# Performance work log

Measured on AMD Instinct MI355X. Metric: run time of the kernel, lower is better.

## Reference

```python
import jax, jax.numpy as jnp
import numpy as np

B = 131072
NUM_KNOTS = 20
X_RANGE = (-5.0, 5.0)
DIMS = [3, 16, 16, 16, 16, 16, 16, 2]
KNOTS = jnp.linspace(X_RANGE[0], X_RANGE[1], NUM_KNOTS, dtype=jnp.float32)


def setup_inputs() -> dict:
    key = jax.random.key(0)
    keys = jax.random.split(key, 2 + 2 * (len(DIMS) - 1))
    inp = {
        "x": jax.random.normal(keys[0], (B, 2), dtype=jnp.float32),
        "t": jax.random.uniform(keys[1], (B, 1), dtype=jnp.float32),
    }
    for l in range(len(DIMS) - 1):
        in_d, out_d = DIMS[l], DIMS[l + 1]
        # per-edge cubic coefficients for each knot interval: [out, in, K-1, 4]
        inp[f"c{l}"] = 0.05 * jax.random.normal(
            keys[2 + 2 * l], (out_d, in_d, NUM_KNOTS - 1, 4), dtype=jnp.float32)
        inp[f"b{l}"] = jnp.zeros((out_d,), dtype=jnp.float32)
    return inp


def kan_layer(x, coeffs, bias):
    """x: [B, in]; coeffs: [out, in, K-1, 4]; bias: [out] -> [B, out].
    Vectorized equivalent of the per-edge CubicSplineFunction double loop:
    bucketize -> gather interval coeffs -> cubic polynomial in dx -> sum over in.
    """
    n_int = coeffs.shape[2]
    idx = jnp.clip(jnp.searchsorted(KNOTS, x, side="right") - 1, 0, n_int - 1)  # [B, in]
    dx = x - KNOTS[idx]                                                          # [B, in]
    dxp = jnp.stack([jnp.ones_like(dx), dx, dx * dx, dx * dx * dx], axis=-1)     # [B, in, 4]
    ii = jnp.arange(x.shape[1])
    cg = coeffs[:, ii[None, :], idx]                                             # [out, B, in, 4]
    return jnp.einsum("obip,bip->bo", cg, dxp) + bias


def reference(x, t, c0, b0, c1, b1, c2, b2, c3, b3, c4, b4, c5, b5, c6, b6):
    cs = [c0, c1, c2, c3, c4, c5, c6]
    bs = [b0, b1, b2, b3, b4, b5, b6]
    h = jnp.concatenate([x, t], axis=1)
    for l in range(len(cs) - 1):
        h = jax.nn.silu(kan_layer(h, cs[l], bs[l]))
    out = kan_layer(h, cs[-1], bs[-1])  # [B, 2]
    return jax.lax.complex(out[..., 0], out[..., 1])
```

## Files before the change

### kernel.cpp

```cpp
#include <hip/hip_runtime.h>
#include <hip/hip_fp16.h>
#include <math.h>


#define B_TOTAL 131072
#define NK 20
#define NI 19

#define W_L0 0
#define W_L1 912
#define W_L6 25232
#define W_TOTAL 25840
#define LSTRIDE 4864

typedef _Float16 h2_t __attribute__((ext_vector_type(2)));

__device__ __forceinline__ h2_t u2h2(unsigned u) {
    union { unsigned u; h2_t h; } c;
    c.u = u;
    return c.h;
}

__device__ __forceinline__ unsigned h2u(h2_t h) {
    union { h2_t h; unsigned u; } c;
    c.h = h;
    return c.u;
}

__device__ __forceinline__ float silu(float a) {
    return a / (1.0f + expf(-a));
}

__device__ __forceinline__ float silu_fast(float a) {
#if __has_builtin(__builtin_amdgcn_rcpf)
    return a * __builtin_amdgcn_rcpf(1.0f + __expf(-a));
#else
    return a / (1.0f + __expf(-a));
#endif
}

__device__ __forceinline__ void find_idx(float v, const float* __restrict__ skp,
                                         int& idx, float& dx) {
    int g0 = (int)floorf((v + 5.0f) * 1.9f);
    g0 = g0 < 0 ? 0 : (g0 > NI - 1 ? NI - 1 : g0);
    const float k0 = skp[g0], k1 = skp[g0 + 1], k2 = skp[g0 + 2];
    int id = g0 - 1; float kk = k0;
    if (v >= k1) { id = g0;     kk = k1; }
    if (v >= k2) { id = g0 + 1; kk = k2; }
    if (id < 0)      { id = 0;      kk = k1; }
    if (id > NI - 1) { id = NI - 1; kk = k1; }
    idx = id; dx = v - kk;
}

#if __has_builtin(__builtin_amdgcn_fdot2)
__device__ __forceinline__ float edge2(unsigned q12, unsigned q03, h2_t dxv,
                                       h2_t onev, float acc) {
    acc = __builtin_amdgcn_fdot2(u2h2(q03), onev, acc, false);
    acc = __builtin_amdgcn_fdot2(u2h2(q12), dxv, acc, false);
    return acc;
}
#else
__device__ __forceinline__ float edge2(unsigned q12, unsigned q03, h2_t dxv,
                                       h2_t onev, float acc) {
    const h2_t a = u2h2(q12), b = u2h2(q03);
    acc += (float)b.x + (float)b.y * (float)onev.y;
    acc += (float)a.x * (float)dxv.x + (float)a.y * (float)dxv.y;
    return acc;
}
#endif

__device__ __forceinline__ float quad_reduce_sum(float v) {
    int t = __builtin_amdgcn_mov_dpp(__float_as_int(v), 0xB1, 0xF, 0xF, true);
    v += __int_as_float(t);
    t = __builtin_amdgcn_mov_dpp(__float_as_int(v), 0x4E, 0xF, 0xF, true);
    v += __int_as_float(t);
    return v;
}

__device__ __forceinline__ void prep_own(float a, const float* __restrict__ skp,
                                         int& mi, unsigned& md, unsigned& mo) {
    const float h = silu_fast(a);
    int idx; float dx;
    find_idx(h, skp, idx, dx);
    const float dx2 = dx * dx, dx3 = dx2 * dx;
    const h2_t dxv = {(_Float16)dx, (_Float16)dx2};
    const h2_t onev = {(_Float16)1.0f, (_Float16)dx3};
    mi = idx; md = h2u(dxv); mo = h2u(onev);
}

template <int HALF>
__device__ __forceinline__ uint4 gl16(const __half* base, unsigned voff) {
    uint4 d;
    if constexpr (HALF == 0)
        asm volatile("global_load_dwordx4 %0, %1, %2 offset:0"
                     : "=v"(d)
                     : "v"(voff), "s"(base));
    else
        asm volatile("global_load_dwordx4 %0, %1, %2 offset:16"
                     : "=v"(d)
                     : "v"(voff), "s"(base));
    return d;
}

#define VM_WAIT_SB(N)                                         \
    do {                                                      \
        asm volatile("s_waitcnt vmcnt(" #N ")" ::: "memory"); \
        __builtin_amdgcn_sched_barrier(0);                    \
    } while (0)

template <int K>
__device__ __forceinline__ void issue_batch(const __half* base, const int* mi,
                                            int q32, uint4* d) {
#pragma unroll
    for (int j = 0; j < 4; ++j) {
        const int idx =
            __builtin_amdgcn_mov_dpp(mi[j], K * 0x55, 0xF, 0xF, true);
        const unsigned voff =
            (unsigned)((((K * 4 + j) * NI + idx) << 7) + q32);
        d[2 * j] = gl16<0>(base, voff);
        d[2 * j + 1] = gl16<1>(base, voff);
    }
}

template <int K>
__device__ __forceinline__ void consume_batch(const uint4* src,
                                              const unsigned* md,
                                              const unsigned* mo, float* acc) {
#pragma unroll
    for (int j = 0; j < 4; ++j) {
        const h2_t dxv = u2h2((unsigned)__builtin_amdgcn_mov_dpp(
            (int)md[j], K * 0x55, 0xF, 0xF, true));
        const h2_t onev = u2h2((unsigned)__builtin_amdgcn_mov_dpp(
            (int)mo[j], K * 0x55, 0xF, 0xF, true));
        const uint4 qa = src[2 * j], qb = src[2 * j + 1];
        acc[0] = edge2(qa.x, qa.y, dxv, onev, acc[0]);
        acc[1] = edge2(qa.z, qa.w, dxv, onev, acc[1]);
        acc[2] = edge2(qb.x, qb.y, dxv, onev, acc[2]);
        acc[3] = edge2(qb.z, qb.w, dxv, onev, acc[3]);
    }
}

__global__ __launch_bounds__(256, 4) void kan_kernel_v6(
    const float* __restrict__ x, const float* __restrict__ t,
    const __half* __restrict__ w, float* __restrict__ out) {
    __shared__ float skp[NK + 1];
    if (threadIdx.x < NK + 1)
        skp[threadIdx.x] =
            (threadIdx.x == 0)
                ? -3.0e38f
                : (float)(-5.0 + (double)(threadIdx.x - 1) * (10.0 / 19.0));
    __syncthreads();

    const int q = threadIdx.x & 3;
    const int q4 = q * 4;
    const int q32 = q4 << 3;
    const int s = blockIdx.x * 64 + (threadIdx.x >> 2);

    const float2 xy = ((const float2*)x)[s];
    const float tv = t[s];

    float acc[4] = {0.f, 0.f, 0.f, 0.f};

    {
        const char* __restrict__ bpq = (const char*)w + q32;
        const float vin[3] = {xy.x, xy.y, tv};
        int i0[3]; unsigned d0[3], o0[3];
#pragma unroll
        for (int i = 0; i < 3; ++i) {
            int idx; float dx;
            find_idx(vin[i], skp, idx, dx);
            const float dx2 = dx * dx, dx3 = dx2 * dx;
            const h2_t dxv = {(_Float16)dx, (_Float16)dx2};
            const h2_t onev = {(_Float16)1.0f, (_Float16)dx3};
            i0[i] = idx; d0[i] = h2u(dxv); o0[i] = h2u(onev);
        }
        uint4 L0[6];
#pragma unroll
        for (int i = 0; i < 3; ++i) {
            const char* p = bpq + (((i * NI) + i0[i]) * 128);
            L0[2 * i] = *(const uint4*)p;
            L0[2 * i + 1] = *(const uint4*)(p + 16);
        }
#pragma unroll
        for (int i = 0; i < 3; ++i) {
            const h2_t dxv = u2h2(d0[i]), onev = u2h2(o0[i]);
            const uint4 qa = L0[2 * i], qb = L0[2 * i + 1];
            acc[0] = edge2(qa.x, qa.y, dxv, onev, acc[0]);
            acc[1] = edge2(qa.z, qa.w, dxv, onev, acc[1]);
            acc[2] = edge2(qb.x, qb.y, dxv, onev, acc[2]);
            acc[3] = edge2(qb.z, qb.w, dxv, onev, acc[3]);
        }
    }

#pragma unroll 1
    for (int l = 0; l < 5; ++l) {
        int mi[4]; unsigned md[4], mo[4];
#pragma unroll
        for (int ii = 0; ii < 4; ++ii)
            prep_own(acc[ii], skp, mi[ii], md[ii], mo[ii]);
#pragma unroll
        for (int j = 0; j < 4; ++j) acc[j] = 0.f;

        const __half* base = w + ((size_t)W_L1 + (size_t)l * LSTRIDE) * 4;

        uint4 b0[8], b1[8], b2[8], b3[8];
        issue_batch<0>(base, mi, q32, b0);
        issue_batch<1>(base, mi, q32, b1);
        VM_WAIT_SB(8);
        consume_batch<0>(b0, md, mo, acc);
        issue_batch<2>(base, mi, q32, b2);
        VM_WAIT_SB(8);
        consume_batch<1>(b1, md, mo, acc);
        issue_batch<3>(base, mi, q32, b3);
        VM_WAIT_SB(8);
        consume_batch<2>(b2, md, mo, acc);
        VM_WAIT_SB(0);
        consume_batch<3>(b3, md, mo, acc);
    }

    {
        const char* __restrict__ c6p = (const char*)w + (size_t)W_L6 * 8;
        int i6[4]; unsigned d6[4], o6[4];
#pragma unroll
        for (int ii = 0; ii < 4; ++ii)
            prep_own(acc[ii], skp, i6[ii], d6[ii], o6[ii]);
        uint4 qv[4];
#pragma unroll
        for (int ii = 0; ii < 4; ++ii)
            qv[ii] = *(const uint4*)(c6p + (((q4 + ii) * NI + i6[ii]) * 16));
        float a0 = 0.f, a1 = 0.f;
#pragma unroll
        for (int ii = 0; ii < 4; ++ii) {
            const h2_t dxv = u2h2(d6[ii]), onev = u2h2(o6[ii]);
            a0 = edge2(qv[ii].x, qv[ii].y, dxv, onev, a0);
            a1 = edge2(qv[ii].z, qv[ii].w, dxv, onev, a1);
        }
        a0 = quad_reduce_sum(a0);
        a1 = quad_reduce_sum(a1);
        if (q == 0) out[s] = a0;
        else if (q == 1) out[B_TOTAL + s] = a1;
    }
}

__global__ __launch_bounds__(256) void repack_kernel(
    const float4* __restrict__ c0, const float4* __restrict__ c1,
    const float4* __restrict__ c2, const float4* __restrict__ c3,
    const float4* __restrict__ c4, const float4* __restrict__ c5,
    const float4* __restrict__ c6, __half* __restrict__ w) {
    const int tid = blockIdx.x * 256 + threadIdx.x;
    if (tid >= W_TOTAL) return;
    const float4* src;
    int IN, OUT, off;
    if (tid < W_L1)                      { src = c0; IN = 3;  OUT = 16; off = W_L0; }
    else if (tid < W_L1 + 1 * LSTRIDE)   { src = c1; IN = 16; OUT = 16; off = W_L1; }
    else if (tid < W_L1 + 2 * LSTRIDE)   { src = c2; IN = 16; OUT = 16; off = W_L1 + 1 * LSTRIDE; }
    else if (tid < W_L1 + 3 * LSTRIDE)   { src = c3; IN = 16; OUT = 16; off = W_L1 + 2 * LSTRIDE; }
    else if (tid < W_L1 + 4 * LSTRIDE)   { src = c4; IN = 16; OUT = 16; off = W_L1 + 3 * LSTRIDE; }
    else if (tid < W_L6)                 { src = c5; IN = 16; OUT = 16; off = W_L1 + 4 * LSTRIDE; }
    else                                 { src = c6; IN = 16; OUT = 2;  off = W_L6; }
    const int d = tid - off;
    const int o = d % OUT;
    const int ik = d / OUT;
    const int k = ik % NI, i = ik / NI;
    const float4 s = src[((size_t)o * IN + i) * NI + k];
    __half* dst = w + (size_t)tid * 4;
    dst[0] = __float2half(s.y);
    dst[1] = __float2half(s.z);
    dst[2] = __float2half(s.x);
    dst[3] = __float2half(s.w);
}

template <int IN, int OUT, bool DO_SILU>
__device__ __forceinline__ void kan_layer_fb(const float* __restrict__ h_in,
                                             float* __restrict__ h_out,
                                             const float4* __restrict__ C,
                                             const float* __restrict__ skp) {
    float acc[OUT];
#pragma unroll
    for (int o = 0; o < OUT; ++o) acc[o] = 0.0f;
#pragma unroll 1
    for (int i = 0; i < IN; ++i) {
        int idx; float dx;
        find_idx(h_in[i], skp, idx, dx);
        const float dx2 = dx * dx, dx3 = dx2 * dx;
        const float4* __restrict__ cp = C + (i * NI + idx);
#pragma unroll
        for (int o = 0; o < OUT; ++o) {
            const float4 c = cp[o * IN * NI];
            acc[o] += fmaf(c.y, dx, fmaf(c.z, dx2, fmaf(c.w, dx3, c.x)));
        }
    }
#pragma unroll
    for (int o = 0; o < OUT; ++o) h_out[o] = DO_SILU ? silu(acc[o]) : acc[o];
}

__global__ __launch_bounds__(256) void kan_kernel_fb(
    const float* __restrict__ x, const float* __restrict__ t,
    const float4* __restrict__ c0, const float4* __restrict__ c1,
    const float4* __restrict__ c2, const float4* __restrict__ c3,
    const float4* __restrict__ c4, const float4* __restrict__ c5,
    const float4* __restrict__ c6, float* __restrict__ out) {
    __shared__ float skp[NK + 1];
    if (threadIdx.x < NK + 1)
        skp[threadIdx.x] =
            (threadIdx.x == 0)
                ? -3.0e38f
                : (float)(-5.0 + (double)(threadIdx.x - 1) * (10.0 / 19.0));
    __syncthreads();
    const int b = blockIdx.x * blockDim.x + threadIdx.x;
    if (b >= B_TOTAL) return;
    const float2 xy = ((const float2*)x)[b];
    float h0[3] = {xy.x, xy.y, t[b]};
    float ha[16], hb[16];
    kan_layer_fb<3, 16, true>(h0, ha, c0, skp);
    kan_layer_fb<16, 16, true>(ha, hb, c1, skp);
    kan_layer_fb<16, 16, true>(hb, ha, c2, skp);
    kan_layer_fb<16, 16, true>(ha, hb, c3, skp);
    kan_layer_fb<16, 16, true>(hb, ha, c4, skp);
    kan_layer_fb<16, 16, true>(ha, hb, c5, skp);
    float ho[2];
    kan_layer_fb<16, 2, false>(hb, ho, c6, skp);
    out[b] = ho[0];
    out[B_TOTAL + b] = ho[1];
}

extern "C" void kernel_launch(void* const* d_in, const int* in_sizes, int n_in,
                              void* d_out, int out_size, void* d_ws, size_t ws_size,
                              hipStream_t stream) {
    const float* x = nullptr;
    const float* t = nullptr;
    const float4* c[7] = {};
    int cmid = 0;
    for (int i = 0; i < n_in; ++i) {
        const int s = in_sizes[i];
        const float* p = (const float*)d_in[i];
        if (s == 262144) x = p;
        else if (s == 131072) t = p;
        else if (s == 3648) c[0] = (const float4*)p;
        else if (s == 19456) { if (cmid < 5) c[1 + cmid++] = (const float4*)p; }
        else if (s == 2432) c[6] = (const float4*)p;
    }

    if (ws_size >= (size_t)W_TOTAL * 8) {
        __half* w = (__half*)d_ws;
        repack_kernel<<<(W_TOTAL + 255) / 256, 256, 0, stream>>>(
            c[0], c[1], c[2], c[3], c[4], c[5], c[6], w);
        kan_kernel_v6<<<B_TOTAL / 64, 256, 0, stream>>>(x, t, w, (float*)d_out);
    } else {
        kan_kernel_fb<<<B_TOTAL / 256, 256, 0, stream>>>(
            x, t, c[0], c[1], c[2], c[3], c[4], c[5], c[6], (float*)d_out);
    }
}
```

Before: 124.3 us.

## Shrink load batches to two edges and double occupancy target

Splits each hidden layer's coefficient gather into eight two-edge batches held in two ping-pong buffers, replacing four four-edge batches in four buffers. Launch bounds now request 8 blocks per SM instead of 4. The aim is to cut VGPR pressure so more waves can hide gather latency. In exchange each wave keeps fewer loads in flight and issues more waitcnt barriers.

```diff
diff --git a/kernel.cpp b/kernel.cpp
--- a/kernel.cpp
+++ b/kernel.cpp
@@ -108,30 +108,30 @@
         __builtin_amdgcn_sched_barrier(0);                    \
     } while (0)
 
-template <int K>
-__device__ __forceinline__ void issue_batch(const __half* base, const int* mi,
-                                            int q32, uint4* d) {
-#pragma unroll
-    for (int j = 0; j < 4; ++j) {
-        const int idx =
-            __builtin_amdgcn_mov_dpp(mi[j], K * 0x55, 0xF, 0xF, true);
+template <int P>
+__device__ __forceinline__ void issue_b2(const __half* base, const int* mi,
+                                         int q32, uint4* d) {
+#pragma unroll
+    for (int j = 0; j < 2; ++j) {
+        const int idx = __builtin_amdgcn_mov_dpp(
+            mi[(P & 1) * 2 + j], (P >> 1) * 0x55, 0xF, 0xF, true);
         const unsigned voff =
-            (unsigned)((((K * 4 + j) * NI + idx) << 7) + q32);
+            (unsigned)((((P * 2 + j) * NI + idx) << 7) + q32);
         d[2 * j] = gl16<0>(base, voff);
         d[2 * j + 1] = gl16<1>(base, voff);
     }
 }
 
-template <int K>
-__device__ __forceinline__ void consume_batch(const uint4* src,
-                                              const unsigned* md,
-                                              const unsigned* mo, float* acc) {
-#pragma unroll
-    for (int j = 0; j < 4; ++j) {
+template <int P>
+__device__ __forceinline__ void consume_b2(const uint4* src,
+                                           const unsigned* md,
+                                           const unsigned* mo, float* acc) {
+#pragma unroll
+    for (int j = 0; j < 2; ++j) {
         const h2_t dxv = u2h2((unsigned)__builtin_amdgcn_mov_dpp(
-            (int)md[j], K * 0x55, 0xF, 0xF, true));
+            (int)md[(P & 1) * 2 + j], (P >> 1) * 0x55, 0xF, 0xF, true));
         const h2_t onev = u2h2((unsigned)__builtin_amdgcn_mov_dpp(
-            (int)mo[j], K * 0x55, 0xF, 0xF, true));
+            (int)mo[(P & 1) * 2 + j], (P >> 1) * 0x55, 0xF, 0xF, true));
         const uint4 qa = src[2 * j], qb = src[2 * j + 1];
         acc[0] = edge2(qa.x, qa.y, dxv, onev, acc[0]);
         acc[1] = edge2(qa.z, qa.w, dxv, onev, acc[1]);
@@ -140,7 +140,7 @@
     }
 }
 
-__global__ __launch_bounds__(256, 4) void kan_kernel_v6(
+__global__ __launch_bounds__(256, 8) void kan_kernel_v7(
     const float* __restrict__ x, const float* __restrict__ t,
     const __half* __restrict__ w, float* __restrict__ out) {
     __shared__ float skp[NK + 1];
@@ -203,19 +203,31 @@
 
         const __half* base = w + ((size_t)W_L1 + (size_t)l * LSTRIDE) * 4;
 
-        uint4 b0[8], b1[8], b2[8], b3[8];
-        issue_batch<0>(base, mi, q32, b0);
-        issue_batch<1>(base, mi, q32, b1);
-        VM_WAIT_SB(8);
-        consume_batch<0>(b0, md, mo, acc);
-        issue_batch<2>(base, mi, q32, b2);
-        VM_WAIT_SB(8);
-        consume_batch<1>(b1, md, mo, acc);
-        issue_batch<3>(base, mi, q32, b3);
-        VM_WAIT_SB(8);
-        consume_batch<2>(b2, md, mo, acc);
+        uint4 bA[4], bB[4];
+        issue_b2<0>(base, mi, q32, bA);
+        issue_b2<1>(base, mi, q32, bB);
+        VM_WAIT_SB(4);
+        consume_b2<0>(bA, md, mo, acc);
+        issue_b2<2>(base, mi, q32, bA);
+        VM_WAIT_SB(4);
+        consume_b2<1>(bB, md, mo, acc);
+        issue_b2<3>(base, mi, q32, bB);
+        VM_WAIT_SB(4);
+        consume_b2<2>(bA, md, mo, acc);
+        issue_b2<4>(base, mi, q32, bA);
+        VM_WAIT_SB(4);
+        consume_b2<3>(bB, md, mo, acc);
+        issue_b2<5>(base, mi, q32, bB);
+        VM_WAIT_SB(4);
+        consume_b2<4>(bA, md, mo, acc);
+        issue_b2<6>(base, mi, q32, bA);
+        VM_WAIT_SB(4);
+        consume_b2<5>(bB, md, mo, acc);
+        issue_b2<7>(base, mi, q32, bB);
+        VM_WAIT_SB(4);
+        consume_b2<6>(bA, md, mo, acc);
         VM_WAIT_SB(0);
-        consume_batch<3>(b3, md, mo, acc);
+        consume_b2<7>(bB, md, mo, acc);
     }
 
     {
@@ -345,7 +357,7 @@
         __half* w = (__half*)d_ws;
         repack_kernel<<<(W_TOTAL + 255) / 256, 256, 0, stream>>>(
             c[0], c[1], c[2], c[3], c[4], c[5], c[6], w);
-        kan_kernel_v6<<<B_TOTAL / 64, 256, 0, stream>>>(x, t, w, (float*)d_out);
+        kan_kernel_v7<<<B_TOTAL / 64, 256, 0, stream>>>(x, t, w, (float*)d_out);
     } else {
         kan_kernel_fb<<<B_TOTAL / 256, 256, 0, stream>>>(
             x, t, c[0], c[1], c[2], c[3], c[4], c[5], c[6], (float*)d_out);
```

New measurement: 132.4 us. +6.5%, slower.

## Shrink load pipeline to double-buffered single-input stages and double occupancy

Applied to the files above, without the earlier changes.

Replaces the four 8-register-deep load batches per hidden layer with a 16-stage ping-pong pipeline that keeps only two 2-load buffers in flight. Launch bounds rise from 4 to 8 waves per EU. The intent is to cut VGPR pressure so more waves can hide global-load latency through occupancy instead of deep per-wave prefetch. The risk is that each wave now has far fewer loads in flight and waits on vmcnt more often, which could expose latency if the extra occupancy does not appear or is not enough.

```diff
diff --git a/kernel.cpp b/kernel.cpp
--- a/kernel.cpp
+++ b/kernel.cpp
@@ -108,39 +108,32 @@
         __builtin_amdgcn_sched_barrier(0);                    \
     } while (0)
 
-template <int K>
-__device__ __forceinline__ void issue_batch(const __half* base, const int* mi,
-                                            int q32, uint4* d) {
-#pragma unroll
-    for (int j = 0; j < 4; ++j) {
-        const int idx =
-            __builtin_amdgcn_mov_dpp(mi[j], K * 0x55, 0xF, 0xF, true);
-        const unsigned voff =
-            (unsigned)((((K * 4 + j) * NI + idx) << 7) + q32);
-        d[2 * j] = gl16<0>(base, voff);
-        d[2 * j + 1] = gl16<1>(base, voff);
-    }
-}
-
-template <int K>
-__device__ __forceinline__ void consume_batch(const uint4* src,
-                                              const unsigned* md,
-                                              const unsigned* mo, float* acc) {
-#pragma unroll
-    for (int j = 0; j < 4; ++j) {
-        const h2_t dxv = u2h2((unsigned)__builtin_amdgcn_mov_dpp(
-            (int)md[j], K * 0x55, 0xF, 0xF, true));
-        const h2_t onev = u2h2((unsigned)__builtin_amdgcn_mov_dpp(
-            (int)mo[j], K * 0x55, 0xF, 0xF, true));
-        const uint4 qa = src[2 * j], qb = src[2 * j + 1];
-        acc[0] = edge2(qa.x, qa.y, dxv, onev, acc[0]);
-        acc[1] = edge2(qa.z, qa.w, dxv, onev, acc[1]);
-        acc[2] = edge2(qb.x, qb.y, dxv, onev, acc[2]);
-        acc[3] = edge2(qb.z, qb.w, dxv, onev, acc[3]);
-    }
-}
-
-__global__ __launch_bounds__(256, 4) void kan_kernel_v6(
+template <int P>
+__device__ __forceinline__ void issue_b1(const __half* base, const int* mi,
+                                         int q32, uint4* d) {
+    const int idx = __builtin_amdgcn_mov_dpp(mi[P & 3], (P >> 2) * 0x55, 0xF,
+                                             0xF, true);
+    const unsigned voff = (unsigned)(((P * NI + idx) << 7) + q32);
+    d[0] = gl16<0>(base, voff);
+    d[1] = gl16<1>(base, voff);
+}
+
+template <int P>
+__device__ __forceinline__ void consume_b1(const uint4* src,
+                                           const unsigned* md,
+                                           const unsigned* mo, float* acc) {
+    const h2_t dxv = u2h2((unsigned)__builtin_amdgcn_mov_dpp(
+        (int)md[P & 3], (P >> 2) * 0x55, 0xF, 0xF, true));
+    const h2_t onev = u2h2((unsigned)__builtin_amdgcn_mov_dpp(
+        (int)mo[P & 3], (P >> 2) * 0x55, 0xF, 0xF, true));
+    const uint4 qa = src[0], qb = src[1];
+    acc[0] = edge2(qa.x, qa.y, dxv, onev, acc[0]);
+    acc[1] = edge2(qa.z, qa.w, dxv, onev, acc[1]);
+    acc[2] = edge2(qb.x, qb.y, dxv, onev, acc[2]);
+    acc[3] = edge2(qb.z, qb.w, dxv, onev, acc[3]);
+}
+
+__global__ __launch_bounds__(256, 8) void kan_kernel_v8(
     const float* __restrict__ x, const float* __restrict__ t,
     const __half* __restrict__ w, float* __restrict__ out) {
     __shared__ float skp[NK + 1];
@@ -203,19 +196,25 @@
 
         const __half* base = w + ((size_t)W_L1 + (size_t)l * LSTRIDE) * 4;
 
-        uint4 b0[8], b1[8], b2[8], b3[8];
-        issue_batch<0>(base, mi, q32, b0);
-        issue_batch<1>(base, mi, q32, b1);
-        VM_WAIT_SB(8);
-        consume_batch<0>(b0, md, mo, acc);
-        issue_batch<2>(base, mi, q32, b2);
-        VM_WAIT_SB(8);
-        consume_batch<1>(b1, md, mo, acc);
-        issue_batch<3>(base, mi, q32, b3);
-        VM_WAIT_SB(8);
-        consume_batch<2>(b2, md, mo, acc);
-        VM_WAIT_SB(0);
-        consume_batch<3>(b3, md, mo, acc);
+        uint4 bA[2], bB[2];
+        issue_b1<0>(base, mi, q32, bA);
+        issue_b1<1>(base, mi, q32, bB);
+        VM_WAIT_SB(2); consume_b1<0>(bA, md, mo, acc);  issue_b1<2>(base, mi, q32, bA);
+        VM_WAIT_SB(2); consume_b1<1>(bB, md, mo, acc);  issue_b1<3>(base, mi, q32, bB);
+        VM_WAIT_SB(2); consume_b1<2>(bA, md, mo, acc);  issue_b1<4>(base, mi, q32, bA);
+        VM_WAIT_SB(2); consume_b1<3>(bB, md, mo, acc);  issue_b1<5>(base, mi, q32, bB);
+        VM_WAIT_SB(2); consume_b1<4>(bA, md, mo, acc);  issue_b1<6>(base, mi, q32, bA);
+        VM_WAIT_SB(2); consume_b1<5>(bB, md, mo, acc);  issue_b1<7>(base, mi, q32, bB);
+        VM_WAIT_SB(2); consume_b1<6>(bA, md, mo, acc);  issue_b1<8>(base, mi, q32, bA);
+        VM_WAIT_SB(2); consume_b1<7>(bB, md, mo, acc);  issue_b1<9>(base, mi, q32, bB);
+        VM_WAIT_SB(2); consume_b1<8>(bA, md, mo, acc);  issue_b1<10>(base, mi, q32, bA);
+        VM_WAIT_SB(2); consume_b1<9>(bB, md, mo, acc);  issue_b1<11>(base, mi, q32, bB);
+        VM_WAIT_SB(2); consume_b1<10>(bA, md, mo, acc); issue_b1<12>(base, mi, q32, bA);
+        VM_WAIT_SB(2); consume_b1<11>(bB, md, mo, acc); issue_b1<13>(base, mi, q32, bB);
+        VM_WAIT_SB(2); consume_b1<12>(bA, md, mo, acc); issue_b1<14>(base, mi, q32, bA);
+        VM_WAIT_SB(2); consume_b1<13>(bB, md, mo, acc); issue_b1<15>(base, mi, q32, bB);
+        VM_WAIT_SB(2); consume_b1<14>(bA, md, mo, acc);
+        VM_WAIT_SB(0); consume_b1<15>(bB, md, mo, acc);
     }
 
     {
@@ -345,7 +344,7 @@
         __half* w = (__half*)d_ws;
         repack_kernel<<<(W_TOTAL + 255) / 256, 256, 0, stream>>>(
             c[0], c[1], c[2], c[3], c[4], c[5], c[6], w);
-        kan_kernel_v6<<<B_TOTAL / 64, 256, 0, stream>>>(x, t, w, (float*)d_out);
+        kan_kernel_v8<<<B_TOTAL / 64, 256, 0, stream>>>(x, t, w, (float*)d_out);
     } else {
         kan_kernel_fb<<<B_TOTAL / 256, 256, 0, stream>>>(
             x, t, c[0], c[1], c[2], c[3], c[4], c[5], c[6], (float*)d_out);
```

Result: no change. 124.9 us (+0.5%).
